# Optimization experiments

Hardware: AMD Instinct MI355X
Metric: run time of the kernel (lower is better)

## Reference

```python
import jax, jax.numpy as jnp
import numpy as np

DIM = 1024
HEADS = 16
HEAD_DIM = DIM // HEADS
WINDOW = 512
NEG = -1e9  # matches masked_fill(-1e9) semantics; excluded keys get ~0 weight


def setup_inputs() -> dict:
    key = jax.random.key(0)
    ks = jax.random.split(key, 9)
    s = 1.0 / np.sqrt(DIM)
    inp = {"x": jax.random.normal(ks[0], (2, 4096, DIM), dtype=jnp.float32)}
    for i, name in enumerate(["q", "k", "v", "o"]):
        inp[f"W{name}"] = jax.random.uniform(ks[1 + 2 * i], (DIM, DIM), jnp.float32, -s, s)
        inp[f"b{name}"] = jax.random.uniform(ks[2 + 2 * i], (DIM,), jnp.float32, -s, s)
    return inp


def _sliding_window_attn(x, Wq, bq, Wk, bk, Wv, bv, Wo, bo):
    B, S, D = x.shape
    H, hd, W = HEADS, HEAD_DIM, WINDOW
    nb = S // W  # number of query blocks

    def proj(Wp, bp):
        y = x @ Wp.T + bp                       # [B,S,D]
        return y.reshape(B, S, H, hd).transpose(0, 2, 1, 3)  # [B,H,S,hd]

    q = proj(Wq, bq)
    k = proj(Wk, bk)
    v = proj(Wv, bv)

    scale = hd ** -0.5
    qb = q.reshape(B, H, nb, W, hd)

    def window_kv(t):
        # each query block n attends to blocks n-1 and n (2W keys)
        pad = jnp.concatenate([jnp.zeros((B, H, W, hd), t.dtype), t], axis=2)
        prev = pad[:, :, :S].reshape(B, H, nb, W, hd)
        cur = t.reshape(B, H, nb, W, hd)
        return jnp.concatenate([prev, cur], axis=3)  # [B,H,nb,2W,hd]

    kw = window_kv(k)
    vw = window_kv(v)

    scores = jnp.einsum('bhnqd,bhnkd->bhnqk', qb, kw) * scale  # [B,H,nb,W,2W]

    # key abs pos = n*W - W + t ; query abs pos = n*W + s
    t = jnp.arange(2 * W)            # [2W]
    s_ = jnp.arange(W)[:, None]      # [W,1]
    n = jnp.arange(nb)[:, None, None]  # [nb,1,1]
    valid = (t <= s_ + W) & (t >= s_ + 1) & (n * W - W + t >= 0)  # [nb,W,2W]
    scores = jnp.where(valid, scores, NEG)

    attn = jax.nn.softmax(scores, axis=-1)
    out = jnp.einsum('bhnqk,bhnkd->bhnqd', attn, vw)  # [B,H,nb,W,hd]
    out = out.reshape(B, H, S, hd).transpose(0, 2, 1, 3).reshape(B, S, D)
    return out @ Wo.T + bo


def reference(x, Wq, bq, Wk, bk, Wv, bv, Wo, bo):
    return _sliding_window_attn(x, Wq, bq, Wk, bk, Wv, bv, Wo, bo)
```

## Files before the change

### kernel.cpp

```cpp
#include <hip/hip_runtime.h>
#include <hip/hip_bf16.h>
#include <cmath>

typedef __bf16 bf16_t;
typedef __attribute__((ext_vector_type(8))) __bf16 bfrag;
typedef __attribute__((ext_vector_type(4))) __bf16 bf16x4;
typedef __attribute__((ext_vector_type(4))) float f32x4;

#define SEQ    4096
#define NDIM   1024
#define NHEAD  16
#define HD     64
#define NBATCH 2
#define MROWS  (NBATCH * SEQ)
#define LQK    2048
#define PSTR   76
#define QSC    0.1803368801111f
#define EXP2(x) exp2f(x)

__device__ __forceinline__ void gload_lds16(const bf16_t* g, bf16_t* l) {
    __builtin_amdgcn_global_load_lds(
        (const __attribute__((address_space(1))) unsigned int*)g,
        (__attribute__((address_space(3))) unsigned int*)l,
        16, 0, 0);
}

__device__ __forceinline__ void block_sync() {
    asm volatile("" ::: "memory");
    __builtin_amdgcn_s_barrier();
    asm volatile("" ::: "memory");
}
#define VMC(n)  asm volatile("s_waitcnt vmcnt(" #n ")" ::: "memory")

__device__ __forceinline__ void stage_half(const bf16_t* __restrict__ G, int ldg,
                                           int grow0, int gk0, bf16_t* region,
                                           int half, int tid)
{
    const int poff = half * 8192 + tid * 16;
    const int loff = poff ^ (((poff >> 9) & 1) << 5);
    const int r    = loff >> 6;
    const int cb   = loff & 63;
    const bf16_t* src = G + (size_t)(grow0 + r) * ldg + gk0 + (cb >> 1);
    gload_lds16(src, region + ((half * 8192 + (tid >> 6) * 1024) >> 1));
}

__device__ __forceinline__ bfrag ldsfrag(const bf16_t* region, int R, int quad)
{
    const int off = (R * 64 + quad * 16) ^ (((R >> 3) & 1) << 5);
    return *(const bfrag*)((const char*)region + off);
}

template <typename OT>
__global__ __launch_bounds__(512, 4)
void gemm2ph(const bf16_t* __restrict__ A, int lda,
             const bf16_t* __restrict__ W,
             const float* __restrict__ b0p, const float* __restrict__ b1p,
             const float* __restrict__ b2p, float qscale,
             OT* __restrict__ C, int ldc, int K,
             bf16_t* __restrict__ VtOut, int nbx)
{
    constexpr int ABUF = 4096;
    constexpr int BBUF = 8192;
    constexpr int BUF  = ABUF + BBUF;
    __shared__ __align__(1024) bf16_t LSD[2 * BUF];

    const int tid  = threadIdx.x;
    const int lane = tid & 63;
    const int n16  = lane & 15;
    const int quad = lane >> 4;
    const int wid  = tid >> 6;
    const int wm   = wid >> 2;
    const int wn   = wid & 3;

    const int nwg = (int)gridDim.x;
    const int f   = (int)blockIdx.x;
    const int swz = (f & 7) * (nwg >> 3) + (f >> 3);
    const int bx  = swz % nbx;
    const int by  = swz / nbx;
    const int row0 = by * 128;
    const int col0 = bx * 256;
    const int nt   = K >> 5;

    f32x4 acc[4][4];
#pragma unroll
    for (int m = 0; m < 4; m++)
#pragma unroll
        for (int j = 0; j < 4; j++) acc[m][j] = (f32x4){0.f, 0.f, 0.f, 0.f};

    {
        bf16_t* A0 = &LSD[0];
        bf16_t* B0 = &LSD[ABUF];
        bf16_t* B1 = &LSD[BUF + ABUF];
        stage_half(A, lda, row0, 0, A0, 0, tid);
        stage_half(W, K, col0, 0, B0, 0, tid);
        stage_half(W, K, col0, 0, B0, 1, tid);
        stage_half(W, K, col0, 32, B1, 0, tid);
        stage_half(W, K, col0, 32, B1, 1, tid);
    }
    VMC(2);

    for (int t = 0; t < nt; ++t) {
        bf16_t* Ab  = &LSD[(t & 1) * BUF];
        bf16_t* Bb  = Ab + ABUF;
        bf16_t* AbN = &LSD[((t & 1) ^ 1) * BUF];

        bfrag a[2], b[4];

        block_sync();
#pragma unroll
        for (int m = 0; m < 2; m++) a[m] = ldsfrag(Ab, wm * 64 + m * 16 + n16, quad);
#pragma unroll
        for (int j = 0; j < 4; j++) b[j] = ldsfrag(Bb, wn * 64 + j * 16 + n16, quad);
        if (t + 1 < nt)
            stage_half(A, lda, row0, (t + 1) * 32, AbN, 0, tid);
        asm volatile("s_waitcnt lgkmcnt(0)" ::: "memory");
        __builtin_amdgcn_sched_barrier(0);
        __builtin_amdgcn_s_setprio(1);
#pragma unroll
        for (int m = 0; m < 2; m++)
#pragma unroll
            for (int j = 0; j < 4; j++)
                acc[m][j] = __builtin_amdgcn_mfma_f32_16x16x32_bf16(a[m], b[j], acc[m][j], 0, 0, 0);
        __builtin_amdgcn_s_setprio(0);

        block_sync();
#pragma unroll
        for (int m = 0; m < 2; m++) a[m] = ldsfrag(Ab, wm * 64 + (m + 2) * 16 + n16, quad);
        if (t + 2 < nt) {
            stage_half(W, K, col0, (t + 2) * 32, Bb, 0, tid);
            stage_half(W, K, col0, (t + 2) * 32, Bb, 1, tid);
        }
        asm volatile("s_waitcnt lgkmcnt(0)" ::: "memory");
        __builtin_amdgcn_sched_barrier(0);
        __builtin_amdgcn_s_setprio(1);
#pragma unroll
        for (int m = 0; m < 2; m++)
#pragma unroll
            for (int j = 0; j < 4; j++)
                acc[m + 2][j] = __builtin_amdgcn_mfma_f32_16x16x32_bf16(a[m], b[j], acc[m + 2][j], 0, 0, 0);
        __builtin_amdgcn_s_setprio(0);

        if (t < nt - 2) { VMC(2); }
        else            { VMC(0); }
    }

    const float* bias = (col0 < 1024) ? b0p : (col0 < 2048 ? b1p : b2p);
    const float bsc   = (col0 < 1024) ? qscale : 1.0f;
    const int bcol0   = col0 & 1023;

    if (col0 < 2048 || VtOut == nullptr) {
#pragma unroll
        for (int m = 0; m < 4; m++)
#pragma unroll
            for (int j = 0; j < 4; j++)
#pragma unroll
                for (int r = 0; r < 4; r++) {
                    int row = row0 + wm * 64 + m * 16 + quad * 4 + r;
                    int col = wn * 64 + j * 16 + n16;
                    float v = acc[m][j][r] + bias[bcol0 + col] * bsc;
                    C[(size_t)row * ldc + col0 + col] = (OT)v;
                }
    } else {
#pragma unroll
        for (int m = 0; m < 4; m++) {
#pragma unroll
            for (int j = 0; j < 4; j++) {
                int dg     = col0 + wn * 64 + j * 16 + n16 - 2048;
                int token0 = row0 + wm * 64 + m * 16 + quad * 4;
                int bb     = token0 >> 12;
                float bv   = bias[bcol0 + wn * 64 + j * 16 + n16];
                size_t vrow = ((size_t)bb * NHEAD + (dg >> 6)) * HD + (dg & 63);
                bf16x4 pk;
#pragma unroll
                for (int r = 0; r < 4; r++) pk[r] = (__bf16)(acc[m][j][r] + bv);
                *(bf16x4*)&VtOut[vrow * SEQ + (token0 & (SEQ - 1))] = pk;
            }
        }
    }
}

__global__ __launch_bounds__(256)
void cast_all(const float* __restrict__ x,
              const float* __restrict__ wq, const float* __restrict__ wk,
              const float* __restrict__ wv, const float* __restrict__ wo,
              bf16_t* __restrict__ dx, bf16_t* __restrict__ dw)
{
    const int bid = (int)blockIdx.x;
    if (bid < 4096) {
        size_t i = ((size_t)bid * 256 + threadIdx.x) * 8;
        float4 a = *(const float4*)(x + i);
        float4 b = *(const float4*)(x + i + 4);
        bfrag o;
        o[0] = (__bf16)a.x; o[1] = (__bf16)a.y; o[2] = (__bf16)a.z; o[3] = (__bf16)a.w;
        o[4] = (__bf16)b.x; o[5] = (__bf16)b.y; o[6] = (__bf16)b.z; o[7] = (__bf16)b.w;
        *(bfrag*)(dx + i) = o;
    } else {
        size_t t   = (size_t)(bid - 4096) * 256 + threadIdx.x;
        int    sel = (int)(t >> 17);
        const float* s = sel == 0 ? wq : (sel == 1 ? wk : (sel == 2 ? wv : wo));
        const float sc = (sel == 0) ? QSC : 1.0f;
        size_t off = (t & 131071) * 8;
        float4 a = *(const float4*)(s + off);
        float4 b = *(const float4*)(s + off + 4);
        bfrag o;
        o[0] = (__bf16)(a.x * sc); o[1] = (__bf16)(a.y * sc);
        o[2] = (__bf16)(a.z * sc); o[3] = (__bf16)(a.w * sc);
        o[4] = (__bf16)(b.x * sc); o[5] = (__bf16)(b.y * sc);
        o[6] = (__bf16)(b.z * sc); o[7] = (__bf16)(b.w * sc);
        *(bfrag*)(dw + (size_t)sel * 1048576 + off) = o;
    }
}

__global__ __launch_bounds__(256, 2)
void attn_win(const bf16_t* __restrict__ QK, const bf16_t* __restrict__ Vt,
              bf16_t* __restrict__ AO)
{
    __shared__ __align__(16) bf16_t Ks[2][64 * 72];
    __shared__ __align__(16) bf16_t Pw[4][32 * PSTR];

    const int tid  = threadIdx.x;
    const int wid  = tid >> 6;
    const int lane = tid & 63;
    const int n16  = lane & 15;
    const int quad = lane >> 4;

    const int lin = blockIdx.x;
    const int sub = lin >> 3;
    const int bh  = (lin & 7) * 4 + (sub >> 5);
    const int qt  = sub & 31;
    const int qb0 = qt * 128;

    const int b  = bh >> 4, h = bh & 15;
    const size_t bS   = (size_t)b * SEQ;
    const size_t hoff = (size_t)h * HD;
    const bf16_t* Vb  = Vt + (size_t)bh * HD * SEQ;
    const int wstart  = qb0 - 512;
    const int it0     = (qb0 < 512) ? ((512 - qb0) >> 6) : 0;

    const int srow  = tid >> 2;
    const int scol0 = (tid & 3) * 16;

    const int qwmin = qb0 + wid * 32;
    const int qwmax = qwmin + 31;
    int qa[2];
    bfrag bq0[2], bq1[2];
#pragma unroll
    for (int qg = 0; qg < 2; qg++) {
        qa[qg] = qwmin + qg * 16 + n16;
        bq0[qg] = *(const bfrag*)(&QK[(bS + qa[qg]) * LQK + hoff + quad * 8]);
        bq1[qg] = *(const bfrag*)(&QK[(bS + qa[qg]) * LQK + hoff + 32 + quad * 8]);
    }

    f32x4 ao[2][4];
#pragma unroll
    for (int qg = 0; qg < 2; qg++)
#pragma unroll
        for (int j = 0; j < 4; j++) ao[qg][j] = (f32x4){0.f, 0.f, 0.f, 0.f};
    float m[2] = {-1e30f, -1e30f}, l[2] = {0.f, 0.f};

    uint4 kp0, kp1;
    {
        const bf16_t* src = &QK[(bS + wstart + it0 * 64 + srow) * LQK + 1024 + hoff + scol0];
        kp0 = *(const uint4*)(src);
        kp1 = *(const uint4*)(src + 8);
    }

    for (int it = it0; it < 10; ++it) {
        const int k0 = wstart + it * 64;
        const int pb = it & 1;
        *(uint4*)(&Ks[pb][srow * 72 + scol0])     = kp0;
        *(uint4*)(&Ks[pb][srow * 72 + scol0 + 8]) = kp1;
        __syncthreads();
        if (it < 9) {
            const bf16_t* src = &QK[(bS + wstart + (it + 1) * 64 + srow) * LQK + 1024 + hoff + scol0];
            kp0 = *(const uint4*)(src);
            kp1 = *(const uint4*)(src + 8);
        }

        if (k0 > qwmax || k0 + 63 < qwmin - 511) continue;

        bfrag vf[2][4];
#pragma unroll
        for (int ks = 0; ks < 2; ks++)
#pragma unroll
            for (int j = 0; j < 4; j++)
                vf[ks][j] = *(const bfrag*)(&Vb[(size_t)(j * 16 + n16) * SEQ
                                                + k0 + ks * 32 + quad * 8]);

        f32x4 a[2][4];
#pragma unroll
        for (int nt = 0; nt < 4; nt++) {
            bfrag ak0 = *(const bfrag*)(&Ks[pb][(nt * 16 + n16) * 72 + quad * 8]);
            bfrag ak1 = *(const bfrag*)(&Ks[pb][(nt * 16 + n16) * 72 + 32 + quad * 8]);
#pragma unroll
            for (int qg = 0; qg < 2; qg++) {
                f32x4 s4 = (f32x4){0.f, 0.f, 0.f, 0.f};
                s4 = __builtin_amdgcn_mfma_f32_16x16x32_bf16(ak0, bq0[qg], s4, 0, 0, 0);
                s4 = __builtin_amdgcn_mfma_f32_16x16x32_bf16(ak1, bq1[qg], s4, 0, 0, 0);
                a[qg][nt] = s4;
            }
        }

#pragma unroll
        for (int qg = 0; qg < 2; qg++) {
            const int gmin = qwmin + qg * 16, gmax = gmin + 15;
            const bool msk = !((k0 >= gmax - 511) & (k0 + 63 <= gmin));
            if (msk) {
#pragma unroll
                for (int nt = 0; nt < 4; nt++)
#pragma unroll
                    for (int r = 0; r < 4; r++) {
                        int ka = k0 + nt * 16 + quad * 4 + r;
                        bool valid = (ka >= qa[qg] - 511) & (ka <= qa[qg]);
                        if (!valid) a[qg][nt][r] = -1e30f;
                    }
            }

            float cm = -1e30f;
#pragma unroll
            for (int nt = 0; nt < 4; nt++)
#pragma unroll
                for (int r = 0; r < 4; r++) cm = fmaxf(cm, a[qg][nt][r]);
            cm = fmaxf(cm, __shfl_xor(cm, 16, 64));
            cm = fmaxf(cm, __shfl_xor(cm, 32, 64));
            if (!__all(cm <= m[qg] + 8.f)) {
                float mn    = fmaxf(m[qg], cm);
                float alpha = EXP2(m[qg] - mn);
                m[qg] = mn;
#pragma unroll
                for (int j = 0; j < 4; j++)
#pragma unroll
                    for (int r = 0; r < 4; r++) ao[qg][j][r] *= alpha;
                l[qg] *= alpha;
            }

            float lacc = 0.f;
#pragma unroll
            for (int nt = 0; nt < 4; nt++) {
                bf16x4 pk;
#pragma unroll
                for (int r = 0; r < 4; r++) {
                    float p = EXP2(a[qg][nt][r] - m[qg]);
                    lacc += p;
                    pk[r] = (__bf16)p;
                }
                *(bf16x4*)&Pw[wid][(qg * 16 + n16) * PSTR + nt * 16 + quad * 4] = pk;
            }
            l[qg] += lacc;
        }

#pragma unroll
        for (int ks = 0; ks < 2; ks++) {
            bfrag bp[2];
#pragma unroll
            for (int qg = 0; qg < 2; qg++)
                bp[qg] = *(const bfrag*)(&Pw[wid][(qg * 16 + n16) * PSTR + ks * 32 + quad * 8]);
#pragma unroll
            for (int j = 0; j < 4; j++) {
#pragma unroll
                for (int qg = 0; qg < 2; qg++)
                    ao[qg][j] = __builtin_amdgcn_mfma_f32_16x16x32_bf16(vf[ks][j], bp[qg], ao[qg][j], 0, 0, 0);
            }
        }
    }

#pragma unroll
    for (int qg = 0; qg < 2; qg++) {
        float lv = l[qg];
        lv += __shfl_xor(lv, 16, 64);
        lv += __shfl_xor(lv, 32, 64);
        const float inv = 1.0f / lv;
#pragma unroll
        for (int j = 0; j < 4; j++) {
            bf16x4 pk;
#pragma unroll
            for (int r = 0; r < 4; r++) pk[r] = (__bf16)(ao[qg][j][r] * inv);
            *(bf16x4*)&AO[(bS + qa[qg]) * NDIM + hoff + j * 16 + quad * 4] = pk;
        }
    }
}

extern "C" void kernel_launch(void* const* d_in, const int* in_sizes, int n_in,
                              void* d_out, int out_size, void* d_ws, size_t ws_size,
                              hipStream_t stream)
{
    const float* x  = (const float*)d_in[0];
    const float* Wq = (const float*)d_in[1];
    const float* bq = (const float*)d_in[2];
    const float* Wk = (const float*)d_in[3];
    const float* bk = (const float*)d_in[4];
    const float* Wv = (const float*)d_in[5];
    const float* bv = (const float*)d_in[6];
    const float* Wo = (const float*)d_in[7];
    const float* bo = (const float*)d_in[8];
    float* out = (float*)d_out;

    const size_t QK_E = (size_t)MROWS * LQK;
    const size_t X_E  = (size_t)MROWS * NDIM;
    if (ws_size < (QK_E + X_E + 4u * 1048576u) * sizeof(bf16_t)) return;

    bf16_t* QKb = (bf16_t*)d_ws;
    bf16_t* AbX = QKb + QK_E;
    bf16_t* Wc  = AbX + X_E;
    bf16_t* Wob = Wc + 3u * 1048576u;
    bf16_t* Vtg = (bf16_t*)d_out;

    cast_all<<<dim3(6144), dim3(256), 0, stream>>>(x, Wq, Wk, Wv, Wo, AbX, Wc);

    gemm2ph<bf16_t><<<dim3(768), dim3(512), 0, stream>>>(
        AbX, NDIM, Wc, bq, bk, bv, QSC, QKb, LQK, NDIM, Vtg, 12);

    attn_win<<<dim3(1024), dim3(256), 0, stream>>>(QKb, Vtg, AbX);

    gemm2ph<float><<<dim3(256), dim3(512), 0, stream>>>(
        AbX, NDIM, Wob, bo, bo, bo, 1.0f, out, NDIM, NDIM, nullptr, 4);
}
```

Before: 236.3 us.

## Load K fragments directly from global memory per wave, dropping LDS staging

Removes the shared-memory double-buffered K tile and its block-wide __syncthreads, so each wave reads its K MFMA fragments straight from global memory (L2/L1), as V already is. This lets each wave skip key tiles independently without block-wide barriers and frees LDS, which may allow higher occupancy. In exchange each wave issues its own redundant global loads of the same K tile (four waves read identical data), and the loads are no longer prefetched one iteration ahead, so latency may be exposed.

```diff
diff --git a/kernel.cpp b/kernel.cpp
--- a/kernel.cpp
+++ b/kernel.cpp
@@ -215,7 +215,6 @@
 void attn_win(const bf16_t* __restrict__ QK, const bf16_t* __restrict__ Vt,
               bf16_t* __restrict__ AO)
 {
-    __shared__ __align__(16) bf16_t Ks[2][64 * 72];
     __shared__ __align__(16) bf16_t Pw[4][32 * PSTR];
 
     const int tid  = threadIdx.x;
@@ -234,11 +233,9 @@
     const size_t bS   = (size_t)b * SEQ;
     const size_t hoff = (size_t)h * HD;
     const bf16_t* Vb  = Vt + (size_t)bh * HD * SEQ;
+    const bf16_t* Kb  = QK + bS * LQK + 1024 + hoff;
     const int wstart  = qb0 - 512;
     const int it0     = (qb0 < 512) ? ((512 - qb0) >> 6) : 0;
-
-    const int srow  = tid >> 2;
-    const int scol0 = (tid & 3) * 16;
 
     const int qwmin = qb0 + wid * 32;
     const int qwmax = qwmin + 31;
@@ -258,27 +255,17 @@
         for (int j = 0; j < 4; j++) ao[qg][j] = (f32x4){0.f, 0.f, 0.f, 0.f};
     float m[2] = {-1e30f, -1e30f}, l[2] = {0.f, 0.f};
 
-    uint4 kp0, kp1;
-    {
-        const bf16_t* src = &QK[(bS + wstart + it0 * 64 + srow) * LQK + 1024 + hoff + scol0];
-        kp0 = *(const uint4*)(src);
-        kp1 = *(const uint4*)(src + 8);
-    }
-
     for (int it = it0; it < 10; ++it) {
         const int k0 = wstart + it * 64;
-        const int pb = it & 1;
-        *(uint4*)(&Ks[pb][srow * 72 + scol0])     = kp0;
-        *(uint4*)(&Ks[pb][srow * 72 + scol0 + 8]) = kp1;
-        __syncthreads();
-        if (it < 9) {
-            const bf16_t* src = &QK[(bS + wstart + (it + 1) * 64 + srow) * LQK + 1024 + hoff + scol0];
-            kp0 = *(const uint4*)(src);
-            kp1 = *(const uint4*)(src + 8);
-        }
-
         if (k0 > qwmax || k0 + 63 < qwmin - 511) continue;
 
+        bfrag ak0[4], ak1[4];
+#pragma unroll
+        for (int nt = 0; nt < 4; nt++) {
+            const bf16_t* kr = Kb + (size_t)(k0 + nt * 16 + n16) * LQK + quad * 8;
+            ak0[nt] = *(const bfrag*)(kr);
+            ak1[nt] = *(const bfrag*)(kr + 32);
+        }
         bfrag vf[2][4];
 #pragma unroll
         for (int ks = 0; ks < 2; ks++)
@@ -290,13 +277,11 @@
         f32x4 a[2][4];
 #pragma unroll
         for (int nt = 0; nt < 4; nt++) {
-            bfrag ak0 = *(const bfrag*)(&Ks[pb][(nt * 16 + n16) * 72 + quad * 8]);
-            bfrag ak1 = *(const bfrag*)(&Ks[pb][(nt * 16 + n16) * 72 + 32 + quad * 8]);
 #pragma unroll
             for (int qg = 0; qg < 2; qg++) {
                 f32x4 s4 = (f32x4){0.f, 0.f, 0.f, 0.f};
-                s4 = __builtin_amdgcn_mfma_f32_16x16x32_bf16(ak0, bq0[qg], s4, 0, 0, 0);
-                s4 = __builtin_amdgcn_mfma_f32_16x16x32_bf16(ak1, bq1[qg], s4, 0, 0, 0);
+                s4 = __builtin_amdgcn_mfma_f32_16x16x32_bf16(ak0[nt], bq0[qg], s4, 0, 0, 0);
+                s4 = __builtin_amdgcn_mfma_f32_16x16x32_bf16(ak1[nt], bq1[qg], s4, 0, 0, 0);
                 a[qg][nt] = s4;
             }
         }
```

Result: slower. 258.5 us (+9.4%).
